# Performance work log

Hardware: AMD Instinct MI355X
Metric: run time of the kernel (lower is better)

## Reference

```python
import jax, jax.numpy as jnp
import numpy as np

B, S, HID, HEADS, FF, NL, SPAN, MAXP, VOCAB = 8, 512, 512, 8, 768, 3, 256, 512, 100
DH = HID // HEADS
EPS = 1e-7  # layer_norm_eps
SCALE = float(np.sqrt(DH * 3.0))  # scale_factor = 1 + len(['p2c','c2p']) = 3


def _ln(x, s, b):
    mu = x.mean(-1, keepdims=True)
    var = ((x - mu) ** 2).mean(-1, keepdims=True)
    return (x - mu) / jnp.sqrt(var + EPS) * s + b


def _rel_bucket(seq_len, bucket=SPAN, max_pos=MAXP):
    # DeBERTa-v2 build_relative_position + make_log_bucket_position (static, numpy)
    ids = np.arange(seq_len)
    rel = ids[:, None] - ids[None, :]
    mid = bucket // 2
    abs_pos = np.where((rel < mid) & (rel > -mid), mid - 1, np.abs(rel)).astype(np.float64)
    log_pos = np.ceil(np.log(abs_pos / mid) / np.log((max_pos - 1) / mid) * (mid - 1)) + mid
    bucket_pos = np.where(abs_pos <= mid, rel.astype(np.float64), log_pos * np.sign(rel))
    return jnp.asarray(bucket_pos.astype(np.int32))  # [S, S]


def setup_inputs():
    key = jax.random.key(0)
    ks = jax.random.split(key, 12)
    w = lambda k, shape: jax.random.normal(k, shape, jnp.float32) * 0.02
    return {
        'image_embeddings': jax.random.normal(ks[0], (B, S, HID), jnp.float32),
        'attention_mask': jnp.ones((B, S), jnp.float32),
        'emb_ln_s': jnp.ones((HID,), jnp.float32), 'emb_ln_b': jnp.zeros((HID,), jnp.float32),
        'rel_emb': w(ks[1], (2 * SPAN, HID)),
        'rel_ln_s': jnp.ones((HID,), jnp.float32), 'rel_ln_b': jnp.zeros((HID,), jnp.float32),
        'Wq': w(ks[2], (NL, HID, HID)), 'bq': jnp.zeros((NL, HID), jnp.float32),
        'Wk': w(ks[3], (NL, HID, HID)), 'bk': jnp.zeros((NL, HID), jnp.float32),
        'Wv': w(ks[4], (NL, HID, HID)), 'bv': jnp.zeros((NL, HID), jnp.float32),
        'Wo': w(ks[5], (NL, HID, HID)), 'bo': jnp.zeros((NL, HID), jnp.float32),
        'attn_ln_s': jnp.ones((NL, HID), jnp.float32), 'attn_ln_b': jnp.zeros((NL, HID), jnp.float32),
        'Wi': w(ks[6], (NL, HID, FF)), 'bi': jnp.zeros((NL, FF), jnp.float32),
        'Wf': w(ks[7], (NL, FF, HID)), 'bf': jnp.zeros((NL, HID), jnp.float32),
        'ffn_ln_s': jnp.ones((NL, HID), jnp.float32), 'ffn_ln_b': jnp.zeros((NL, HID), jnp.float32),
        'Wc': w(ks[8], (HID, VOCAB)), 'bc': jnp.zeros((VOCAB,), jnp.float32),
    }


def reference(image_embeddings, attention_mask, emb_ln_s, emb_ln_b, rel_emb, rel_ln_s, rel_ln_b,
              Wq, bq, Wk, bk, Wv, bv, Wo, bo, attn_ln_s, attn_ln_b,
              Wi, bi, Wf, bf, ffn_ln_s, ffn_ln_b, Wc, bc):
    b, s, hid = image_embeddings.shape
    rel = _rel_bucket(s)
    c2p_idx = jnp.clip(rel + SPAN, 0, 2 * SPAN - 1)[None, None]   # [1,1,S,S]
    p2c_idx = jnp.clip(-rel + SPAN, 0, 2 * SPAN - 1)[None, None]  # [1,1,S,S]

    # embeddings: LayerNorm(inputs_embeds) * mask (position_biased_input=False)
    h = _ln(image_embeddings, emb_ln_s, emb_ln_b) * attention_mask[:, :, None]
    rel_e = _ln(rel_emb, rel_ln_s, rel_ln_b)  # norm_rel_ebd='layer_norm'
    m = (attention_mask[:, None, :, None] * attention_mask[:, None, None, :]) > 0  # [B,1,S,S]
    neg = jnp.finfo(h.dtype).min

    for l in range(NL):
        q = (h @ Wq[l] + bq[l]).reshape(b, s, HEADS, DH)
        k = (h @ Wk[l] + bk[l]).reshape(b, s, HEADS, DH)
        v = (h @ Wv[l] + bv[l]).reshape(b, s, HEADS, DH)
        scores = jnp.einsum('bqhd,bkhd->bhqk', q, k) / SCALE
        # share_att_key=True: pos projections reuse key/query projections
        pk = (rel_e @ Wk[l] + bk[l]).reshape(2 * SPAN, HEADS, DH)
        pq = (rel_e @ Wq[l] + bq[l]).reshape(2 * SPAN, HEADS, DH)
        # content-to-position
        c2p = jnp.einsum('bqhd,rhd->bhqr', q, pk)  # [B,H,S,2*SPAN]
        c2p = jnp.take_along_axis(c2p, c2p_idx, axis=-1)  # [B,H,S,S]
        # position-to-content (gather along last dim, then transpose q/k)
        p2c = jnp.einsum('bkhd,rhd->bhkr', k, pq)  # [B,H,S,2*SPAN]
        p2c = jnp.take_along_axis(p2c, p2c_idx, axis=-1).transpose(0, 1, 3, 2)  # [B,H,S,S]
        scores = scores + c2p / SCALE + p2c / SCALE
        # XSoftmax: mask -> -inf, softmax, re-zero masked probs
        probs = jax.nn.softmax(jnp.where(m, scores, neg), axis=-1)
        probs = jnp.where(m, probs, 0.0)
        ctx = jnp.einsum('bhqk,bkhd->bqhd', probs, v).reshape(b, s, hid)
        h = _ln(ctx @ Wo[l] + bo[l] + h, attn_ln_s[l], attn_ln_b[l])
        f = jax.nn.gelu(h @ Wi[l] + bi[l], approximate=False)
        h = _ln(f @ Wf[l] + bf[l] + h, ffn_ln_s[l], ffn_ln_b[l])

    return h @ Wc + bc  # token-classification logits [B,S,VOCAB]
```

## Files before the change

### kernel.cpp

```cpp
#include <hip/hip_runtime.h>
#include <hip/hip_bf16.h>
#include <math.h>

#define EPS_LN 1e-7f
#define INV_SCALE 0.072168783648703221f
#define NEGMAX -3.402823466e38f

typedef unsigned short u16;
typedef __attribute__((ext_vector_type(8))) short bf16x8;
typedef __attribute__((ext_vector_type(4))) float f32x4;

__device__ __forceinline__ u16 f2b(float f) {
  union { float f; unsigned int u; } v; v.f = f;
  unsigned int r = v.u + 0x7FFFu + ((v.u >> 16) & 1u);
  return (u16)(r >> 16);
}
__device__ __forceinline__ float b2f(u16 u) {
  union { unsigned int u; float f; } v; v.u = ((unsigned int)u) << 16;
  return v.f;
}
__device__ __forceinline__ float gelu_exact(float v) {
  return 0.5f * v * (1.f + erff(v * 0.70710678118654752440f));
}

__global__ __launch_bounds__(256) void relbucket_kernel(int* __restrict__ crel) {
  int idx = blockIdx.x * 256 + threadIdx.x;
  if (idx >= 1023) return;
  int rel = idx - 511;
  int a = (rel < 128 && rel > -128) ? 127 : (rel < 0 ? -rel : rel);
  int bucket;
  if (a <= 128) {
    bucket = rel;
  } else {
    double lp = ceil(log((double)a / 128.0) / log(511.0 / 128.0) * 127.0) + 128.0;
    int l = (int)lp;
    bucket = (rel > 0) ? l : -l;
  }
  int c = bucket + 256;
  c = c < 0 ? 0 : (c > 511 ? 511 : c);
  crel[idx] = c;
}

__global__ __launch_bounds__(256) void biascat_kernel(const float* __restrict__ bq,
                                                      const float* __restrict__ bk,
                                                      const float* __restrict__ bv,
                                                      float* __restrict__ o) {
  int i = blockIdx.x * 256 + threadIdx.x;
  if (i >= 4608) return;
  int l = i / 1536, c = i - l * 1536;
  float v = (c < 512) ? bq[l * 512 + c]
                      : (c < 1024) ? bk[l * 512 + c - 512] : bv[l * 512 + c - 1024];
  o[i] = v;
}

template <bool RESID, bool MASK>
__global__ __launch_bounds__(256) void ln_kernel(const float* __restrict__ x,
                                                 const float* __restrict__ res,
                                                 const float* __restrict__ gam,
                                                 const float* __restrict__ bet,
                                                 const float* __restrict__ mask,
                                                 float* __restrict__ out,
                                                 u16* __restrict__ outb, int nrows) {
  int w = threadIdx.x >> 6, ln = threadIdx.x & 63;
  int row = blockIdx.x * 4 + w;
  if (row >= nrows) return;
  const float* xr = x + (size_t)row * 512;
  float v[8];
#pragma unroll
  for (int c = 0; c < 2; ++c) {
    float4 a = *(const float4*)(xr + (ln << 3) + (c << 2));
    v[c * 4 + 0] = a.x; v[c * 4 + 1] = a.y; v[c * 4 + 2] = a.z; v[c * 4 + 3] = a.w;
    if (RESID) {
      float4 r4 = *(const float4*)(res + (size_t)row * 512 + (ln << 3) + (c << 2));
      v[c * 4 + 0] += r4.x; v[c * 4 + 1] += r4.y; v[c * 4 + 2] += r4.z; v[c * 4 + 3] += r4.w;
    }
  }
  float sum = 0.f;
#pragma unroll
  for (int c = 0; c < 8; ++c) sum += v[c];
#pragma unroll
  for (int off = 32; off; off >>= 1) sum += __shfl_xor(sum, off);
  float mu = sum * (1.f / 512.f);
  float vs = 0.f;
#pragma unroll
  for (int c = 0; c < 8; ++c) { float d = v[c] - mu; vs += d * d; }
#pragma unroll
  for (int off = 32; off; off >>= 1) vs += __shfl_xor(vs, off);
  float rstd = 1.f / sqrtf(vs * (1.f / 512.f) + EPS_LN);
  float mk = MASK ? mask[row] : 1.f;
  float* orow = out + (size_t)row * 512;
  u16* brow = outb ? outb + (size_t)row * 512 : nullptr;
#pragma unroll
  for (int c = 0; c < 2; ++c) {
    int col = (ln << 3) + (c << 2);
    float o[4];
#pragma unroll
    for (int q = 0; q < 4; ++q)
      o[q] = ((v[c * 4 + q] - mu) * rstd * gam[col + q] + bet[col + q]) * mk;
    *(float4*)(orow + col) = make_float4(o[0], o[1], o[2], o[3]);
    if (brow) {
      ushort4 ob = { f2b(o[0]), f2b(o[1]), f2b(o[2]), f2b(o[3]) };
      *(ushort4*)(brow + col) = ob;
    }
  }
}

__global__ __launch_bounds__(256) void wtrans_kernel(const float* __restrict__ W,
                                                     u16* __restrict__ Wt,
                                                     int K, int N, long wstride, long tstride) {
  __shared__ float tl[32][33];
  int z = blockIdx.z;
  W += (size_t)z * wstride;
  Wt += (size_t)z * tstride;
  int n0 = blockIdx.x * 32, k0 = blockIdx.y * 32;
  int c = threadIdx.x & 31, r8 = threadIdx.x >> 5;
#pragma unroll
  for (int p = 0; p < 4; ++p) {
    int r = r8 + p * 8;
    int k = k0 + r, n = n0 + c;
    tl[r][c] = (k < K && n < N) ? W[(size_t)k * N + n] : 0.f;
  }
  __syncthreads();
#pragma unroll
  for (int p = 0; p < 4; ++p) {
    int r = r8 + p * 8;
    int n = n0 + r, k = k0 + c;
    if (n < N && k < K) Wt[(size_t)n * K + k] = f2b(tl[c][r]);
  }
}

__global__ __launch_bounds__(256) void vtrans_kernel(const u16* __restrict__ qkv,
                                                     u16* __restrict__ vT) {
  __shared__ u16 tl[32][33];
  int z = blockIdx.z;
  int b = z >> 3, h = z & 7;
  int j0 = blockIdx.x * 32, d0 = blockIdx.y * 32;
  int c = threadIdx.x & 31, r8 = threadIdx.x >> 5;
#pragma unroll
  for (int p = 0; p < 4; ++p) {
    int r = r8 + p * 8;
    tl[r][c] = qkv[(size_t)(b * 512 + j0 + r) * 1536 + 1024 + h * 64 + d0 + c];
  }
  __syncthreads();
#pragma unroll
  for (int p = 0; p < 4; ++p) {
    int r = r8 + p * 8;
    vT[(size_t)z * 32768 + (size_t)(d0 + r) * 512 + j0 + c] = tl[c][r];
  }
}

template <int EPI, typename CT>
__global__ __launch_bounds__(256) void gemm128(const u16* __restrict__ A,
                                               const u16* __restrict__ B,
                                               const float* __restrict__ bias,
                                               CT* __restrict__ C,
                                               int M, int N, int K,
                                               int lda, int ldb, int ldc) {
  __shared__ u16 As[128][72];
  __shared__ u16 Bs[64][72];
  int t = threadIdx.x;
  int m0 = blockIdx.y * 128, n0 = blockIdx.x * 64;
  int w = t >> 6, l = t & 63;
  int wr = w >> 1, wc = w & 1, lr = l & 15, kg = l >> 4;
  f32x4 acc[4][2] = {};
  for (int k0 = 0; k0 < K; k0 += 64) {
#pragma unroll
    for (int p = 0; p < 4; ++p) {
      int c = t + (p << 8);
      int row = c >> 3, q = c & 7;
      *(uint4*)(&As[row][q * 8]) =
          *(const uint4*)(A + (size_t)(m0 + row) * lda + k0 + q * 8);
    }
#pragma unroll
    for (int p = 0; p < 2; ++p) {
      int c = t + (p << 8);
      int row = c >> 3, q = c & 7;
      *(uint4*)(&Bs[row][q * 8]) =
          *(const uint4*)(B + (size_t)(n0 + row) * ldb + k0 + q * 8);
    }
    __syncthreads();
#pragma unroll
    for (int s = 0; s < 2; ++s) {
      bf16x8 a[4], bb[2];
#pragma unroll
      for (int m = 0; m < 4; ++m)
        a[m] = *(const bf16x8*)(&As[wr * 64 + m * 16 + lr][kg * 8 + s * 32]);
#pragma unroll
      for (int n = 0; n < 2; ++n)
        bb[n] = *(const bf16x8*)(&Bs[wc * 32 + n * 16 + lr][kg * 8 + s * 32]);
#pragma unroll
      for (int m = 0; m < 4; ++m)
#pragma unroll
        for (int n = 0; n < 2; ++n)
          acc[m][n] = __builtin_amdgcn_mfma_f32_16x16x32_bf16(a[m], bb[n], acc[m][n], 0, 0, 0);
    }
    __syncthreads();
  }
#pragma unroll
  for (int m = 0; m < 4; ++m)
#pragma unroll
    for (int n = 0; n < 2; ++n) {
      int col = n0 + wc * 32 + n * 16 + lr;
      float bv = (EPI >= 1) ? bias[col] : 0.f;
#pragma unroll
      for (int r = 0; r < 4; ++r) {
        int row = m0 + wr * 64 + m * 16 + kg * 4 + r;
        float v = acc[m][n][r] + bv;
        if (EPI == 2) v = gelu_exact(v);
        if constexpr (sizeof(CT) == 2) {
          ((u16*)C)[(size_t)row * ldc + col] = f2b(v);
        } else {
          ((float*)C)[(size_t)row * ldc + col] = v;
        }
      }
    }
}

template <int EPI, typename CT>
__global__ __launch_bounds__(256) void gemm_bf16(const u16* __restrict__ A,
                                                 const u16* __restrict__ B,
                                                 const float* __restrict__ bias,
                                                 CT* __restrict__ C,
                                                 int M, int N, int K,
                                                 int lda, int ldb, int ldc,
                                                 long sAb, long sAh, long sBb, long sBh,
                                                 long sCb, long sCh) {
  __shared__ u16 As[64][72];
  __shared__ u16 Bs[64][72];
  int t = threadIdx.x;
  int z = blockIdx.z, zb = z >> 3, zh = z & 7;
  A += (size_t)zb * sAb + (size_t)zh * sAh;
  B += (size_t)zb * sBb + (size_t)zh * sBh;
  C += (size_t)zb * sCb + (size_t)zh * sCh;
  int m0 = blockIdx.y * 64, n0 = blockIdx.x * 64;
  int w = t >> 6, l = t & 63;
  int wr = w >> 1, wc = w & 1, lr = l & 15, kg = l >> 4;
  f32x4 acc[2][2] = {};
  for (int k0 = 0; k0 < K; k0 += 64) {
#pragma unroll
    for (int p = 0; p < 2; ++p) {
      int c = t + (p << 8);
      int row = c >> 3, q = c & 7;
      uint4 av = *(const uint4*)(A + (size_t)(m0 + row) * lda + k0 + q * 8);
      *(uint4*)(&As[row][q * 8]) = av;
      uint4 bv = make_uint4(0u, 0u, 0u, 0u);
      if (n0 + row < N) bv = *(const uint4*)(B + (size_t)(n0 + row) * ldb + k0 + q * 8);
      *(uint4*)(&Bs[row][q * 8]) = bv;
    }
    __syncthreads();
#pragma unroll
    for (int s = 0; s < 2; ++s) {
      bf16x8 a0 = *(const bf16x8*)(&As[wr * 32 + lr][kg * 8 + s * 32]);
      bf16x8 a1 = *(const bf16x8*)(&As[wr * 32 + 16 + lr][kg * 8 + s * 32]);
      bf16x8 b0 = *(const bf16x8*)(&Bs[wc * 32 + lr][kg * 8 + s * 32]);
      bf16x8 b1 = *(const bf16x8*)(&Bs[wc * 32 + 16 + lr][kg * 8 + s * 32]);
      acc[0][0] = __builtin_amdgcn_mfma_f32_16x16x32_bf16(a0, b0, acc[0][0], 0, 0, 0);
      acc[0][1] = __builtin_amdgcn_mfma_f32_16x16x32_bf16(a0, b1, acc[0][1], 0, 0, 0);
      acc[1][0] = __builtin_amdgcn_mfma_f32_16x16x32_bf16(a1, b0, acc[1][0], 0, 0, 0);
      acc[1][1] = __builtin_amdgcn_mfma_f32_16x16x32_bf16(a1, b1, acc[1][1], 0, 0, 0);
    }
    __syncthreads();
  }
#pragma unroll
  for (int m = 0; m < 2; ++m)
#pragma unroll
    for (int n = 0; n < 2; ++n) {
      int col = n0 + wc * 32 + n * 16 + lr;
      if (col < N) {
        float bv = (EPI >= 1) ? bias[col] : 0.f;
#pragma unroll
        for (int r = 0; r < 4; ++r) {
          int row = m0 + wr * 32 + m * 16 + kg * 4 + r;
          float v = acc[m][n][r] + bv;
          if (EPI == 2) v = gelu_exact(v);
          if constexpr (sizeof(CT) == 2) {
            ((u16*)C)[(size_t)row * ldc + col] = f2b(v);
          } else {
            ((float*)C)[(size_t)row * ldc + col] = v;
          }
        }
      }
    }
}

__global__ __launch_bounds__(256) void attn_fused(const u16* __restrict__ qkv,
                                                  const u16* __restrict__ vT,
                                                  const u16* __restrict__ Qpk,
                                                  const u16* __restrict__ KpqT,
                                                  const float* __restrict__ mask,
                                                  const int* __restrict__ crel,
                                                  u16* __restrict__ po,
                                                  float* __restrict__ pms) {
  __shared__ u16 ks[64][72];
  __shared__ u16 vs[64][72];
  __shared__ u16 kpq_s[128][72];
  __shared__ u16 crl16[1024];
  int t = threadIdx.x;
  int it = blockIdx.x;
  int z = blockIdx.y;
  int js = blockIdx.z;
  int b = z >> 3, h = z & 7;
  int i0 = it * 64;
  int w = t >> 6, l = t & 63;
  int lr = l & 15, kg = l >> 4;

  for (int c = t; c < 1023; c += 256) crl16[c] = (u16)crel[c];

  const u16* qrow = qkv + (size_t)(b * 512 + i0 + w * 16 + lr) * 1536 + h * 64;
  bf16x8 qa0 = *(const bf16x8*)(qrow + kg * 8);
  bf16x8 qa1 = *(const bf16x8*)(qrow + kg * 8 + 32);

  float m_run[4], s_run[4];
  f32x4 o[4] = {};
  float mi[4];
#pragma unroll
  for (int r = 0; r < 4; ++r) {
    m_run[r] = NEGMAX;
    s_run[r] = 0.f;
    mi[r] = mask[b * 512 + i0 + w * 16 + kg * 4 + r];
  }
  const u16* qpk_base = Qpk + (size_t)z * 262144;
  const u16* kpq_base = KpqT + (size_t)z * 327680;
  __syncthreads();

  for (int jj = 0; jj < 2; ++jj) {
    int j0 = (js * 2 + jj) * 64;
    int idx_base = crl16[i0 - j0 - 63 + 511];
    __syncthreads();
    for (int c = t; c < 512; c += 256) {
      int row = c >> 3, off = (c & 7) * 8;
      *(uint4*)(&ks[row][off]) =
          *(const uint4*)(qkv + (size_t)(b * 512 + j0 + row) * 1536 + 512 + h * 64 + off);
      *(uint4*)(&vs[row][off]) =
          *(const uint4*)(vT + (size_t)z * 32768 + (size_t)row * 512 + j0 + off);
    }
    for (int c = t; c < 1024; c += 256) {
      int row = c >> 3, off = (c & 7) * 8;
      *(uint4*)(&kpq_s[row][off]) =
          *(const uint4*)(kpq_base + (size_t)(idx_base + row) * 512 + j0 + off);
    }
    __syncthreads();
    f32x4 sc[4];
#pragma unroll
    for (int nf = 0; nf < 4; ++nf) {
      bf16x8 kb0 = *(const bf16x8*)(&ks[nf * 16 + lr][kg * 8]);
      bf16x8 kb1 = *(const bf16x8*)(&ks[nf * 16 + lr][kg * 8 + 32]);
      f32x4 a = {};
      a = __builtin_amdgcn_mfma_f32_16x16x32_bf16(qa0, kb0, a, 0, 0, 0);
      a = __builtin_amdgcn_mfma_f32_16x16x32_bf16(qa1, kb1, a, 0, 0, 0);
      sc[nf] = a;
    }
    float mj[4];
#pragma unroll
    for (int nf = 0; nf < 4; ++nf) mj[nf] = mask[b * 512 + j0 + nf * 16 + lr];
    float lgv[4][4];
    bool ok[4][4];
    float tmax[4] = {NEGMAX, NEGMAX, NEGMAX, NEGMAX};
    int iloc = w * 16 + kg * 4;
#pragma unroll
    for (int nf = 0; nf < 4; ++nf) {
      int jloc = nf * 16 + lr;
      int relc = i0 + iloc - (j0 + jloc) + 511;
#pragma unroll
      for (int r = 0; r < 4; ++r) {
        int idx = crl16[relc + r];
        float bias = b2f(qpk_base[(size_t)(i0 + iloc + r) * 512 + idx]) +
                     b2f(kpq_s[idx - idx_base][jloc]);
        bool o_ = (mi[r] * mj[nf]) > 0.f;
        float v = o_ ? (sc[nf][r] + bias) * INV_SCALE : NEGMAX;
        ok[nf][r] = o_;
        lgv[nf][r] = v;
        tmax[r] = fmaxf(tmax[r], v);
      }
    }
#pragma unroll
    for (int r = 0; r < 4; ++r) {
#pragma unroll
      for (int off = 8; off; off >>= 1) tmax[r] = fmaxf(tmax[r], __shfl_xor(tmax[r], off));
    }
    float tsum[4];
#pragma unroll
    for (int r = 0; r < 4; ++r) {
      float mn = fmaxf(m_run[r], tmax[r]);
      float scale = (mn <= -1e37f) ? 1.f : __expf(m_run[r] - mn);
      m_run[r] = mn;
      s_run[r] *= scale;
      o[0][r] *= scale; o[1][r] *= scale; o[2][r] *= scale; o[3][r] *= scale;
      float ls = 0.f;
#pragma unroll
      for (int nf = 0; nf < 4; ++nf) {
        float p = ok[nf][r] ? __expf(lgv[nf][r] - mn) : 0.f;
        lgv[nf][r] = p;
        ls += p;
      }
      tsum[r] = ls;
    }
#pragma unroll
    for (int r = 0; r < 4; ++r) {
#pragma unroll
      for (int off = 8; off; off >>= 1) tsum[r] += __shfl_xor(tsum[r], off);
      s_run[r] += tsum[r];
    }
    __syncthreads();
#pragma unroll
    for (int nf = 0; nf < 4; ++nf)
#pragma unroll
      for (int r = 0; r < 4; ++r) ks[w * 16 + kg * 4 + r][nf * 16 + lr] = f2b(lgv[nf][r]);
    bf16x8 pa0 = *(const bf16x8*)(&ks[w * 16 + lr][kg * 8]);
    bf16x8 pa1 = *(const bf16x8*)(&ks[w * 16 + lr][kg * 8 + 32]);
#pragma unroll
    for (int nf = 0; nf < 4; ++nf) {
      bf16x8 vb0 = *(const bf16x8*)(&vs[nf * 16 + lr][kg * 8]);
      bf16x8 vb1 = *(const bf16x8*)(&vs[nf * 16 + lr][kg * 8 + 32]);
      o[nf] = __builtin_amdgcn_mfma_f32_16x16x32_bf16(pa0, vb0, o[nf], 0, 0, 0);
      o[nf] = __builtin_amdgcn_mfma_f32_16x16x32_bf16(pa1, vb1, o[nf], 0, 0, 0);
    }
  }
#pragma unroll
  for (int r = 0; r < 4; ++r) {
    int i = i0 + w * 16 + kg * 4 + r;
    size_t pb = (((size_t)js * 64 + z) * 512 + i) * 64;
#pragma unroll
    for (int nf = 0; nf < 4; ++nf) po[pb + nf * 16 + lr] = f2b(o[nf][r]);
    if (lr == 0) {
      size_t mb = (((size_t)js * 64 + z) * 512 + i) * 2;
      pms[mb + 0] = m_run[r];
      pms[mb + 1] = s_run[r];
    }
  }
}

__global__ __launch_bounds__(256) void merge_kernel(const u16* __restrict__ po,
                                                    const float* __restrict__ pms,
                                                    u16* __restrict__ ctx) {
  int t = threadIdx.x;
  int w = t >> 6, d = t & 63;
  int row = blockIdx.x * 4 + w;
  int z = row >> 9, i = row & 511;
  int b = z >> 3, h = z & 7;
  float mv[4], sv[4], m = NEGMAX;
#pragma unroll
  for (int js = 0; js < 4; ++js) {
    size_t mb = (((size_t)js * 64 + z) * 512 + i) * 2;
    mv[js] = pms[mb + 0];
    sv[js] = pms[mb + 1];
    m = fmaxf(m, mv[js]);
  }
  float o = 0.f, s = 0.f;
#pragma unroll
  for (int js = 0; js < 4; ++js) {
    float wgt = (mv[js] <= -1e37f) ? 0.f : __expf(mv[js] - m);
    o += wgt * b2f(po[(((size_t)js * 64 + z) * 512 + i) * 64 + d]);
    s += wgt * sv[js];
  }
  float r = (s > 0.f) ? o / s : 0.f;
  ctx[(size_t)(b * 512 + i) * 512 + h * 64 + d] = f2b(r);
}

extern "C" void kernel_launch(void* const* d_in, const int* in_sizes, int n_in,
                              void* d_out, int out_size, void* d_ws, size_t ws_size,
                              hipStream_t stream) {
  const float* x       = (const float*)d_in[0];
  const float* mask    = (const float*)d_in[1];
  const float* emb_s   = (const float*)d_in[2];
  const float* emb_b   = (const float*)d_in[3];
  const float* rel_emb = (const float*)d_in[4];
  const float* rel_s   = (const float*)d_in[5];
  const float* rel_b   = (const float*)d_in[6];
  const float* Wq = (const float*)d_in[7];
  const float* bq = (const float*)d_in[8];
  const float* Wk = (const float*)d_in[9];
  const float* bk = (const float*)d_in[10];
  const float* Wv = (const float*)d_in[11];
  const float* bv = (const float*)d_in[12];
  const float* Wo = (const float*)d_in[13];
  const float* bo = (const float*)d_in[14];
  const float* as_ = (const float*)d_in[15];
  const float* ab_ = (const float*)d_in[16];
  const float* Wi = (const float*)d_in[17];
  const float* bi = (const float*)d_in[18];
  const float* Wf = (const float*)d_in[19];
  const float* bf_ = (const float*)d_in[20];
  const float* fs_ = (const float*)d_in[21];
  const float* fb_ = (const float*)d_in[22];
  const float* Wc = (const float*)d_in[23];
  const float* bc = (const float*)d_in[24];
  float* out = (float*)d_out;

  char* p = (char*)d_ws;
  auto alloc = [&](size_t bytes) {
    char* r = p;
    p += (bytes + 255) & ~(size_t)255;
    return r;
  };
  float* hcat = (float*)alloc((size_t)4608 * 512 * 4);
  float* tmpA = (float*)alloc((size_t)4096 * 512 * 4);
  u16* mid  = (u16*)alloc((size_t)4096 * 768 * 2);
  u16* hbf  = (u16*)alloc((size_t)4608 * 512 * 2);
  u16* po   = (u16*)tmpA;
  float* pms = (float*)((char*)tmpA + (size_t)4 * 64 * 512 * 64 * 2);
  u16* qkv  = (u16*)alloc((size_t)4608 * 1536 * 2);
  u16* vT   = (u16*)alloc((size_t)64 * 64 * 512 * 2);
  u16* ctxb = (u16*)alloc((size_t)4096 * 512 * 2);
  u16* WtQKV = (u16*)alloc((size_t)3 * 1536 * 512 * 2);
  u16* WtO  = (u16*)alloc((size_t)3 * 512 * 512 * 2);
  u16* WtI  = (u16*)alloc((size_t)3 * 768 * 512 * 2);
  u16* WtF  = (u16*)alloc((size_t)3 * 512 * 768 * 2);
  u16* WtC  = (u16*)alloc((size_t)100 * 512 * 2);
  float* bqkv = (float*)alloc((size_t)3 * 1536 * 4);
  u16* Qpk  = (u16*)alloc((size_t)64 * 512 * 512 * 2);
  u16* KpqT = (u16*)alloc((size_t)64 * 640 * 512 * 2);
  int* crel = (int*)alloc((size_t)1024 * 4);

  relbucket_kernel<<<4, 256, 0, stream>>>(crel);
  biascat_kernel<<<18, 256, 0, stream>>>(bq, bk, bv, bqkv);
  wtrans_kernel<<<dim3(16, 16, 3), 256, 0, stream>>>(Wq, WtQKV, 512, 512, 262144, 786432);
  wtrans_kernel<<<dim3(16, 16, 3), 256, 0, stream>>>(Wk, WtQKV + 262144, 512, 512, 262144, 786432);
  wtrans_kernel<<<dim3(16, 16, 3), 256, 0, stream>>>(Wv, WtQKV + 524288, 512, 512, 262144, 786432);
  wtrans_kernel<<<dim3(16, 16, 3), 256, 0, stream>>>(Wo, WtO, 512, 512, 262144, 262144);
  wtrans_kernel<<<dim3(24, 16, 3), 256, 0, stream>>>(Wi, WtI, 512, 768, 393216, 393216);
  wtrans_kernel<<<dim3(16, 24, 3), 256, 0, stream>>>(Wf, WtF, 768, 512, 393216, 393216);
  wtrans_kernel<<<dim3(4, 16, 1), 256, 0, stream>>>(Wc, WtC, 512, 100, 0, 0);
  ln_kernel<false, true><<<1024, 256, 0, stream>>>(x, nullptr, emb_s, emb_b, mask,
                                                   hcat, hbf, 4096);
  ln_kernel<false, false><<<128, 256, 0, stream>>>(rel_emb, nullptr, rel_s, rel_b, nullptr,
                                                   hcat + (size_t)4096 * 512,
                                                   hbf + (size_t)4096 * 512, 512);

  for (int l = 0; l < 3; ++l) {
    gemm128<1, u16><<<dim3(24, 36), 256, 0, stream>>>(
        hbf, WtQKV + (size_t)l * 786432, bqkv + l * 1536, qkv,
        4608, 1536, 512, 512, 512, 1536);
    vtrans_kernel<<<dim3(16, 2, 64), 256, 0, stream>>>(qkv, vT);
    gemm_bf16<0, u16><<<dim3(8, 8, 64), 256, 0, stream>>>(
        qkv, qkv + (size_t)4096 * 1536 + 512, nullptr, Qpk, 512, 512, 64,
        1536, 1536, 512, 786432, 64, 0, 64, 2097152, 262144);
    gemm_bf16<0, u16><<<dim3(8, 8, 64), 256, 0, stream>>>(
        qkv + (size_t)4096 * 1536, qkv + 512, nullptr, KpqT, 512, 512, 64,
        1536, 1536, 512, 0, 64, 786432, 64, 2621440, 327680);
    attn_fused<<<dim3(8, 64, 4), 256, 0, stream>>>(qkv, vT, Qpk, KpqT, mask, crel,
                                                   po, pms);
    merge_kernel<<<8192, 256, 0, stream>>>(po, pms, ctxb);
    gemm128<1, float><<<dim3(8, 32), 256, 0, stream>>>(
        ctxb, WtO + (size_t)l * 262144, bo + l * 512, tmpA, 4096, 512, 512, 512, 512, 512);
    ln_kernel<true, false><<<1024, 256, 0, stream>>>(tmpA, hcat, as_ + l * 512, ab_ + l * 512,
                                                     nullptr, hcat, hbf, 4096);
    gemm128<2, u16><<<dim3(12, 32), 256, 0, stream>>>(
        hbf, WtI + (size_t)l * 393216, bi + l * 768, mid, 4096, 768, 512, 512, 512, 768);
    gemm128<1, float><<<dim3(8, 32), 256, 0, stream>>>(
        mid, WtF + (size_t)l * 393216, bf_ + l * 512, tmpA, 4096, 512, 768, 768, 768, 512);
    ln_kernel<true, false><<<1024, 256, 0, stream>>>(tmpA, hcat, fs_ + l * 512, fb_ + l * 512,
                                                     nullptr, hcat, hbf, 4096);
  }
  gemm_bf16<1, float><<<dim3(2, 64, 1), 256, 0, stream>>>(
      hbf, WtC, bc, out, 4096, 100, 512, 512, 512, 100, 0, 0, 0, 0, 0, 0);
}
```

Baseline: 520.4 us.

## Compute relative-position bias tiles inside attention instead of materializing Qpk/KpqT

Drops the two batched GEMMs that wrote full c2p (Qpk) and p2c (KpqT) matrices to global memory. The attention kernel now computes only the 128-bucket window of relative-position scores each 64x64 tile needs, using MFMA on the projected relative embeddings staged in shared memory. The key dimension is split into 8 single-tile blocks instead of 4 two-tile blocks, so the online-softmax loop goes away and merge_kernel combines 8 partials. This removes large global writes and reads of the bias matrices, at the cost of redundant per-tile MFMA work, a larger partial buffer and a heavier merge.

```diff
diff --git a/kernel.cpp b/kernel.cpp
--- a/kernel.cpp
+++ b/kernel.cpp
@@ -222,16 +222,10 @@
                                                  const float* __restrict__ bias,
                                                  CT* __restrict__ C,
                                                  int M, int N, int K,
-                                                 int lda, int ldb, int ldc,
-                                                 long sAb, long sAh, long sBb, long sBh,
-                                                 long sCb, long sCh) {
+                                                 int lda, int ldb, int ldc) {
   __shared__ u16 As[64][72];
   __shared__ u16 Bs[64][72];
   int t = threadIdx.x;
-  int z = blockIdx.z, zb = z >> 3, zh = z & 7;
-  A += (size_t)zb * sAb + (size_t)zh * sAh;
-  B += (size_t)zb * sBb + (size_t)zh * sBh;
-  C += (size_t)zb * sCb + (size_t)zh * sCh;
   int m0 = blockIdx.y * 64, n0 = blockIdx.x * 64;
   int w = t >> 6, l = t & 63;
   int wr = w >> 1, wc = w & 1, lr = l & 15, kg = l >> 4;
@@ -285,136 +279,163 @@
 
 __global__ __launch_bounds__(256) void attn_fused(const u16* __restrict__ qkv,
                                                   const u16* __restrict__ vT,
-                                                  const u16* __restrict__ Qpk,
-                                                  const u16* __restrict__ KpqT,
                                                   const float* __restrict__ mask,
                                                   const int* __restrict__ crel,
                                                   u16* __restrict__ po,
                                                   float* __restrict__ pms) {
   __shared__ u16 ks[64][72];
-  __shared__ u16 vs[64][72];
-  __shared__ u16 kpq_s[128][72];
+  __shared__ u16 U1[128][72];
+  __shared__ u16 U2[128][72];
   __shared__ u16 crl16[1024];
   int t = threadIdx.x;
   int it = blockIdx.x;
   int z = blockIdx.y;
   int js = blockIdx.z;
   int b = z >> 3, h = z & 7;
-  int i0 = it * 64;
+  int i0 = it * 64, j0 = js * 64;
   int w = t >> 6, l = t & 63;
   int lr = l & 15, kg = l >> 4;
 
   for (int c = t; c < 1023; c += 256) crl16[c] = (u16)crel[c];
+  __syncthreads();
+  int ib = crl16[i0 - j0 - 63 + 511];
+
+  for (int c = t; c < 512; c += 256) {
+    int row = c >> 3, off = (c & 7) * 8;
+    *(uint4*)(&ks[row][off]) =
+        *(const uint4*)(qkv + (size_t)(b * 512 + j0 + row) * 1536 + 512 + h * 64 + off);
+  }
+  for (int c = t; c < 1024; c += 256) {
+    int row = c >> 3, off = (c & 7) * 8;
+    int rw = ib + row;
+    rw = rw > 511 ? 511 : rw;
+    const u16* relrow = qkv + (size_t)(4096 + rw) * 1536 + h * 64;
+    *(uint4*)(&U1[row][off]) = *(const uint4*)(relrow + 512 + off);
+    *(uint4*)(&U2[row][off]) = *(const uint4*)(relrow + off);
+  }
 
   const u16* qrow = qkv + (size_t)(b * 512 + i0 + w * 16 + lr) * 1536 + h * 64;
   bf16x8 qa0 = *(const bf16x8*)(qrow + kg * 8);
   bf16x8 qa1 = *(const bf16x8*)(qrow + kg * 8 + 32);
-
-  float m_run[4], s_run[4];
+  __syncthreads();
+
+  f32x4 sc[4];
+#pragma unroll
+  for (int nf = 0; nf < 4; ++nf) {
+    bf16x8 kb0 = *(const bf16x8*)(&ks[nf * 16 + lr][kg * 8]);
+    bf16x8 kb1 = *(const bf16x8*)(&ks[nf * 16 + lr][kg * 8 + 32]);
+    f32x4 a = {};
+    a = __builtin_amdgcn_mfma_f32_16x16x32_bf16(qa0, kb0, a, 0, 0, 0);
+    a = __builtin_amdgcn_mfma_f32_16x16x32_bf16(qa1, kb1, a, 0, 0, 0);
+    sc[nf] = a;
+  }
+  f32x4 b1a[8];
+#pragma unroll
+  for (int f = 0; f < 8; ++f) {
+    bf16x8 p0 = *(const bf16x8*)(&U1[f * 16 + lr][kg * 8]);
+    bf16x8 p1 = *(const bf16x8*)(&U1[f * 16 + lr][kg * 8 + 32]);
+    f32x4 a = {};
+    a = __builtin_amdgcn_mfma_f32_16x16x32_bf16(qa0, p0, a, 0, 0, 0);
+    a = __builtin_amdgcn_mfma_f32_16x16x32_bf16(qa1, p1, a, 0, 0, 0);
+    b1a[f] = a;
+  }
+  f32x4 b2a[2][4];
+#pragma unroll
+  for (int g = 0; g < 2; ++g) {
+    bf16x8 a0 = *(const bf16x8*)(&U2[w * 32 + g * 16 + lr][kg * 8]);
+    bf16x8 a1 = *(const bf16x8*)(&U2[w * 32 + g * 16 + lr][kg * 8 + 32]);
+#pragma unroll
+    for (int f = 0; f < 4; ++f) {
+      bf16x8 kb0 = *(const bf16x8*)(&ks[f * 16 + lr][kg * 8]);
+      bf16x8 kb1 = *(const bf16x8*)(&ks[f * 16 + lr][kg * 8 + 32]);
+      f32x4 a = {};
+      a = __builtin_amdgcn_mfma_f32_16x16x32_bf16(a0, kb0, a, 0, 0, 0);
+      a = __builtin_amdgcn_mfma_f32_16x16x32_bf16(a1, kb1, a, 0, 0, 0);
+      b2a[g][f] = a;
+    }
+  }
+  __syncthreads();
+  u16* b1 = &U1[0][0];
+#pragma unroll
+  for (int f = 0; f < 8; ++f)
+#pragma unroll
+    for (int r = 0; r < 4; ++r)
+      b1[(w * 16 + kg * 4 + r) * 136 + f * 16 + lr] = f2b(b1a[f][r]);
+#pragma unroll
+  for (int g = 0; g < 2; ++g)
+#pragma unroll
+    for (int f = 0; f < 4; ++f)
+#pragma unroll
+      for (int r = 0; r < 4; ++r)
+        U2[w * 32 + g * 16 + kg * 4 + r][f * 16 + lr] = f2b(b2a[g][f][r]);
+  __syncthreads();
+
+  bf16x8 vb[4][2];
+#pragma unroll
+  for (int nf = 0; nf < 4; ++nf) {
+    const u16* vrow = vT + (size_t)z * 32768 + (size_t)(nf * 16 + lr) * 512 + j0;
+    vb[nf][0] = *(const bf16x8*)(vrow + kg * 8);
+    vb[nf][1] = *(const bf16x8*)(vrow + kg * 8 + 32);
+  }
+
+  float mi[4], mj[4];
+#pragma unroll
+  for (int r = 0; r < 4; ++r) mi[r] = mask[b * 512 + i0 + w * 16 + kg * 4 + r];
+#pragma unroll
+  for (int nf = 0; nf < 4; ++nf) mj[nf] = mask[b * 512 + j0 + nf * 16 + lr];
+  float lgv[4][4];
+  bool ok[4][4];
+  float tmax[4] = {NEGMAX, NEGMAX, NEGMAX, NEGMAX};
+  int iloc = w * 16 + kg * 4;
+#pragma unroll
+  for (int nf = 0; nf < 4; ++nf) {
+    int jloc = nf * 16 + lr;
+    int relc = i0 + iloc - (j0 + jloc) + 511;
+#pragma unroll
+    for (int r = 0; r < 4; ++r) {
+      int idx = crl16[relc + r] - ib;
+      float bias = b2f(b1[(iloc + r) * 136 + idx]) + b2f(U2[idx][jloc]);
+      bool o_ = (mi[r] * mj[nf]) > 0.f;
+      float v = o_ ? (sc[nf][r] + bias) * INV_SCALE : NEGMAX;
+      ok[nf][r] = o_;
+      lgv[nf][r] = v;
+      tmax[r] = fmaxf(tmax[r], v);
+    }
+  }
+#pragma unroll
+  for (int r = 0; r < 4; ++r) {
+#pragma unroll
+    for (int off = 8; off; off >>= 1) tmax[r] = fmaxf(tmax[r], __shfl_xor(tmax[r], off));
+  }
+  float tsum[4];
+#pragma unroll
+  for (int r = 0; r < 4; ++r) {
+    float mn = tmax[r];
+    float ls = 0.f;
+#pragma unroll
+    for (int nf = 0; nf < 4; ++nf) {
+      float p = ok[nf][r] ? __expf(lgv[nf][r] - mn) : 0.f;
+      lgv[nf][r] = p;
+      ls += p;
+    }
+    tsum[r] = ls;
+  }
+#pragma unroll
+  for (int r = 0; r < 4; ++r) {
+#pragma unroll
+    for (int off = 8; off; off >>= 1) tsum[r] += __shfl_xor(tsum[r], off);
+  }
+#pragma unroll
+  for (int nf = 0; nf < 4; ++nf)
+#pragma unroll
+    for (int r = 0; r < 4; ++r) ks[w * 16 + kg * 4 + r][nf * 16 + lr] = f2b(lgv[nf][r]);
+  bf16x8 pa0 = *(const bf16x8*)(&ks[w * 16 + lr][kg * 8]);
+  bf16x8 pa1 = *(const bf16x8*)(&ks[w * 16 + lr][kg * 8 + 32]);
   f32x4 o[4] = {};
-  float mi[4];
-#pragma unroll
-  for (int r = 0; r < 4; ++r) {
-    m_run[r] = NEGMAX;
-    s_run[r] = 0.f;
-    mi[r] = mask[b * 512 + i0 + w * 16 + kg * 4 + r];
-  }
-  const u16* qpk_base = Qpk + (size_t)z * 262144;
-  const u16* kpq_base = KpqT + (size_t)z * 327680;
-  __syncthreads();
-
-  for (int jj = 0; jj < 2; ++jj) {
-    int j0 = (js * 2 + jj) * 64;
-    int idx_base = crl16[i0 - j0 - 63 + 511];
-    __syncthreads();
-    for (int c = t; c < 512; c += 256) {
-      int row = c >> 3, off = (c & 7) * 8;
-      *(uint4*)(&ks[row][off]) =
-          *(const uint4*)(qkv + (size_t)(b * 512 + j0 + row) * 1536 + 512 + h * 64 + off);
-      *(uint4*)(&vs[row][off]) =
-          *(const uint4*)(vT + (size_t)z * 32768 + (size_t)row * 512 + j0 + off);
-    }
-    for (int c = t; c < 1024; c += 256) {
-      int row = c >> 3, off = (c & 7) * 8;
-      *(uint4*)(&kpq_s[row][off]) =
-          *(const uint4*)(kpq_base + (size_t)(idx_base + row) * 512 + j0 + off);
-    }
-    __syncthreads();
-    f32x4 sc[4];
-#pragma unroll
-    for (int nf = 0; nf < 4; ++nf) {
-      bf16x8 kb0 = *(const bf16x8*)(&ks[nf * 16 + lr][kg * 8]);
-      bf16x8 kb1 = *(const bf16x8*)(&ks[nf * 16 + lr][kg * 8 + 32]);
-      f32x4 a = {};
-      a = __builtin_amdgcn_mfma_f32_16x16x32_bf16(qa0, kb0, a, 0, 0, 0);
-      a = __builtin_amdgcn_mfma_f32_16x16x32_bf16(qa1, kb1, a, 0, 0, 0);
-      sc[nf] = a;
-    }
-    float mj[4];
-#pragma unroll
-    for (int nf = 0; nf < 4; ++nf) mj[nf] = mask[b * 512 + j0 + nf * 16 + lr];
-    float lgv[4][4];
-    bool ok[4][4];
-    float tmax[4] = {NEGMAX, NEGMAX, NEGMAX, NEGMAX};
-    int iloc = w * 16 + kg * 4;
-#pragma unroll
-    for (int nf = 0; nf < 4; ++nf) {
-      int jloc = nf * 16 + lr;
-      int relc = i0 + iloc - (j0 + jloc) + 511;
-#pragma unroll
-      for (int r = 0; r < 4; ++r) {
-        int idx = crl16[relc + r];
-        float bias = b2f(qpk_base[(size_t)(i0 + iloc + r) * 512 + idx]) +
-                     b2f(kpq_s[idx - idx_base][jloc]);
-        bool o_ = (mi[r] * mj[nf]) > 0.f;
-        float v = o_ ? (sc[nf][r] + bias) * INV_SCALE : NEGMAX;
-        ok[nf][r] = o_;
-        lgv[nf][r] = v;
-        tmax[r] = fmaxf(tmax[r], v);
-      }
-    }
-#pragma unroll
-    for (int r = 0; r < 4; ++r) {
-#pragma unroll
-      for (int off = 8; off; off >>= 1) tmax[r] = fmaxf(tmax[r], __shfl_xor(tmax[r], off));
-    }
-    float tsum[4];
-#pragma unroll
-    for (int r = 0; r < 4; ++r) {
-      float mn = fmaxf(m_run[r], tmax[r]);
-      float scale = (mn <= -1e37f) ? 1.f : __expf(m_run[r] - mn);
-      m_run[r] = mn;
-      s_run[r] *= scale;
-      o[0][r] *= scale; o[1][r] *= scale; o[2][r] *= scale; o[3][r] *= scale;
-      float ls = 0.f;
-#pragma unroll
-      for (int nf = 0; nf < 4; ++nf) {
-        float p = ok[nf][r] ? __expf(lgv[nf][r] - mn) : 0.f;
-        lgv[nf][r] = p;
-        ls += p;
-      }
-      tsum[r] = ls;
-    }
-#pragma unroll
-    for (int r = 0; r < 4; ++r) {
-#pragma unroll
-      for (int off = 8; off; off >>= 1) tsum[r] += __shfl_xor(tsum[r], off);
-      s_run[r] += tsum[r];
-    }
-    __syncthreads();
-#pragma unroll
-    for (int nf = 0; nf < 4; ++nf)
-#pragma unroll
-      for (int r = 0; r < 4; ++r) ks[w * 16 + kg * 4 + r][nf * 16 + lr] = f2b(lgv[nf][r]);
-    bf16x8 pa0 = *(const bf16x8*)(&ks[w * 16 + lr][kg * 8]);
-    bf16x8 pa1 = *(const bf16x8*)(&ks[w * 16 + lr][kg * 8 + 32]);
-#pragma unroll
-    for (int nf = 0; nf < 4; ++nf) {
-      bf16x8 vb0 = *(const bf16x8*)(&vs[nf * 16 + lr][kg * 8]);
-      bf16x8 vb1 = *(const bf16x8*)(&vs[nf * 16 + lr][kg * 8 + 32]);
-      o[nf] = __builtin_amdgcn_mfma_f32_16x16x32_bf16(pa0, vb0, o[nf], 0, 0, 0);
-      o[nf] = __builtin_amdgcn_mfma_f32_16x16x32_bf16(pa1, vb1, o[nf], 0, 0, 0);
-    }
+#pragma unroll
+  for (int nf = 0; nf < 4; ++nf) {
+    o[nf] = __builtin_amdgcn_mfma_f32_16x16x32_bf16(pa0, vb[nf][0], o[nf], 0, 0, 0);
+    o[nf] = __builtin_amdgcn_mfma_f32_16x16x32_bf16(pa1, vb[nf][1], o[nf], 0, 0, 0);
   }
 #pragma unroll
   for (int r = 0; r < 4; ++r) {
@@ -424,8 +445,8 @@
     for (int nf = 0; nf < 4; ++nf) po[pb + nf * 16 + lr] = f2b(o[nf][r]);
     if (lr == 0) {
       size_t mb = (((size_t)js * 64 + z) * 512 + i) * 2;
-      pms[mb + 0] = m_run[r];
-      pms[mb + 1] = s_run[r];
+      pms[mb + 0] = tmax[r];
+      pms[mb + 1] = tsum[r];
     }
   }
 }
@@ -438,9 +459,9 @@
   int row = blockIdx.x * 4 + w;
   int z = row >> 9, i = row & 511;
   int b = z >> 3, h = z & 7;
-  float mv[4], sv[4], m = NEGMAX;
-#pragma unroll
-  for (int js = 0; js < 4; ++js) {
+  float mv[8], sv[8], m = NEGMAX;
+#pragma unroll
+  for (int js = 0; js < 8; ++js) {
     size_t mb = (((size_t)js * 64 + z) * 512 + i) * 2;
     mv[js] = pms[mb + 0];
     sv[js] = pms[mb + 1];
@@ -448,7 +469,7 @@
   }
   float o = 0.f, s = 0.f;
 #pragma unroll
-  for (int js = 0; js < 4; ++js) {
+  for (int js = 0; js < 8; ++js) {
     float wgt = (mv[js] <= -1e37f) ? 0.f : __expf(mv[js] - m);
     o += wgt * b2f(po[(((size_t)js * 64 + z) * 512 + i) * 64 + d]);
     s += wgt * sv[js];
@@ -497,19 +518,17 @@
   float* tmpA = (float*)alloc((size_t)4096 * 512 * 4);
   u16* mid  = (u16*)alloc((size_t)4096 * 768 * 2);
   u16* hbf  = (u16*)alloc((size_t)4608 * 512 * 2);
-  u16* po   = (u16*)tmpA;
-  float* pms = (float*)((char*)tmpA + (size_t)4 * 64 * 512 * 64 * 2);
   u16* qkv  = (u16*)alloc((size_t)4608 * 1536 * 2);
   u16* vT   = (u16*)alloc((size_t)64 * 64 * 512 * 2);
   u16* ctxb = (u16*)alloc((size_t)4096 * 512 * 2);
+  u16* po   = (u16*)alloc((size_t)8 * 64 * 512 * 64 * 2);
+  float* pms = (float*)alloc((size_t)8 * 64 * 512 * 2 * 4);
   u16* WtQKV = (u16*)alloc((size_t)3 * 1536 * 512 * 2);
   u16* WtO  = (u16*)alloc((size_t)3 * 512 * 512 * 2);
   u16* WtI  = (u16*)alloc((size_t)3 * 768 * 512 * 2);
   u16* WtF  = (u16*)alloc((size_t)3 * 512 * 768 * 2);
   u16* WtC  = (u16*)alloc((size_t)100 * 512 * 2);
   float* bqkv = (float*)alloc((size_t)3 * 1536 * 4);
-  u16* Qpk  = (u16*)alloc((size_t)64 * 512 * 512 * 2);
-  u16* KpqT = (u16*)alloc((size_t)64 * 640 * 512 * 2);
   int* crel = (int*)alloc((size_t)1024 * 4);
 
   relbucket_kernel<<<4, 256, 0, stream>>>(crel);
@@ -532,14 +551,7 @@
         hbf, WtQKV + (size_t)l * 786432, bqkv + l * 1536, qkv,
         4608, 1536, 512, 512, 512, 1536);
     vtrans_kernel<<<dim3(16, 2, 64), 256, 0, stream>>>(qkv, vT);
-    gemm_bf16<0, u16><<<dim3(8, 8, 64), 256, 0, stream>>>(
-        qkv, qkv + (size_t)4096 * 1536 + 512, nullptr, Qpk, 512, 512, 64,
-        1536, 1536, 512, 786432, 64, 0, 64, 2097152, 262144);
-    gemm_bf16<0, u16><<<dim3(8, 8, 64), 256, 0, stream>>>(
-        qkv + (size_t)4096 * 1536, qkv + 512, nullptr, KpqT, 512, 512, 64,
-        1536, 1536, 512, 0, 64, 786432, 64, 2621440, 327680);
-    attn_fused<<<dim3(8, 64, 4), 256, 0, stream>>>(qkv, vT, Qpk, KpqT, mask, crel,
-                                                   po, pms);
+    attn_fused<<<dim3(8, 64, 8), 256, 0, stream>>>(qkv, vT, mask, crel, po, pms);
     merge_kernel<<<8192, 256, 0, stream>>>(po, pms, ctxb);
     gemm128<1, float><<<dim3(8, 32), 256, 0, stream>>>(
         ctxb, WtO + (size_t)l * 262144, bo + l * 512, tmpA, 4096, 512, 512, 512, 512, 512);
@@ -552,6 +564,6 @@
     ln_kernel<true, false><<<1024, 256, 0, stream>>>(tmpA, hcat, fs_ + l * 512, fb_ + l * 512,
                                                      nullptr, hcat, hbf, 4096);
   }
-  gemm_bf16<1, float><<<dim3(2, 64, 1), 256, 0, stream>>>(
-      hbf, WtC, bc, out, 4096, 100, 512, 512, 512, 100, 0, 0, 0, 0, 0, 0);
-}
+  gemm_bf16<1, float><<<dim3(2, 64), 256, 0, stream>>>(
+      hbf, WtC, bc, out, 4096, 100, 512, 512, 512, 100);
+}
```

Result: faster. 482.8 us (-7.2%).
